# Performance work log

Measured on AMD Instinct MI355X. Metric: run time of the kernel, lower is better.

## Reference

```python
import jax, jax.numpy as jnp
import numpy as np

# Baked genome DAG structure (static per-instance in the original module)
N_IN = 256
LAYER_SIZES = [256, 256, 256, 256, 64]  # 4 hidden layers + output layer
N_OUT = LAYER_SIZES[-1]
N_EVAL = sum(LAYER_SIZES)  # 1088 eval nodes (node_evals)
DEG = 32                   # incoming links per eval node
BATCH = 8192


def setup_inputs() -> dict:
    key = jax.random.key(0)
    kx, kw, kb, kr = jax.random.split(key, 4)
    x = jax.random.normal(kx, (BATCH, N_IN), dtype=jnp.float32)
    # connection weights, node bias, node response (learned genome params)
    w = jax.random.normal(kw, (N_EVAL, DEG), dtype=jnp.float32) * 0.5
    bias = jax.random.normal(kb, (N_EVAL,), dtype=jnp.float32) * 0.1
    response = 1.0 + jax.random.normal(kr, (N_EVAL,), dtype=jnp.float32) * 0.1
    # per-layer source indices: each eval node connects to DEG earlier nodes
    src_rows = []
    offset = N_IN  # number of nodes topologically before current layer
    for li, sz in enumerate(LAYER_SIZES):
        ks = jax.random.fold_in(key, 100 + li)
        src_rows.append(jax.random.randint(ks, (sz, DEG), 0, offset, dtype=jnp.int32))
        offset += sz
    src_idx = jnp.concatenate(src_rows, axis=0)  # [N_EVAL, DEG]
    return {"x": x, "w": w, "bias": bias, "response": response, "src_idx": src_idx}


def reference(x, w, bias, response, src_idx):
    # values: [B, n_nodes_so_far]; starts as the input node values
    values = x
    row = 0
    for sz in LAYER_SIZES:  # small fixed structural loop (topological layers)
        s = src_idx[row:row + sz]                       # [sz, DEG]
        gathered = values[:, s]                         # [B, sz, DEG]
        agg = jnp.einsum('bsd,sd->bs', gathered, w[row:row + sz])  # sum aggregation
        out = jax.nn.relu(bias[row:row + sz] + response[row:row + sz] * agg)
        values = jnp.concatenate([values, out], axis=1)
        row += sz
    return values[:, -N_OUT:]  # [B, N_OUT]
```

## Files before the change

kernel.cpp:

```cpp
#include <hip/hip_runtime.h>

#define N_IN   256
#define N_EVAL 1088
#define TOTALW 1344
#define DEG    32

typedef __attribute__((ext_vector_type(8))) short short8;
typedef __attribute__((ext_vector_type(4))) float f32x4;
typedef unsigned short u16;
typedef unsigned int   u32;

__device__ __forceinline__ u32 pk2(float lo, float hi) {
    u32 ul = __float_as_uint(lo);
    u32 uh = __float_as_uint(hi);
    ul = (ul + 0x7fffu + ((ul >> 16) & 1u)) >> 16;
    uh = (uh + 0x7fffu + ((uh >> 16) & 1u)) & 0xffff0000u;
    return ul | uh;
}
__device__ __forceinline__ u16 bf1(float v) {
    u32 u = __float_as_uint(v);
    return (u16)((u + 0x7fffu + ((u >> 16) & 1u)) >> 16);
}

__global__ __launch_bounds__(256) void build_dense32(
    const int* __restrict__ src, const float* __restrict__ w,
    u32* __restrict__ B32)
{
    const int t = blockIdx.x * 256 + threadIdx.x;
    const int tile = t >> 8;
    const int q    = t & 255;
    const int lane = q >> 2;
    const int e2   = q & 3;
    int li, ts;
    if      (tile < 128)  { li = 0; ts = 0;    }
    else if (tile < 384)  { li = 1; ts = 128;  }
    else if (tile < 768)  { li = 2; ts = 384;  }
    else if (tile < 1280) { li = 3; ts = 768;  }
    else                  { li = 4; ts = 1280; }
    const int tloc = tile - ts;
    int kt, nt;
    if (li < 4) { kt = tloc >> 4; nt = tloc & 15; }
    else        { kt = tloc >> 2; nt = tloc & 3;  }
    const int ln = lane & 15, g = lane >> 4;
    const int gn = li * 256 + nt * 16 + ln;
    const int k0 = kt * 32 + g * 8 + e2 * 2;

    int c[DEG]; float ow[DEG];
    const int4*   s4 = (const int4*)(src + (size_t)gn * DEG);
    const float4* w4 = (const float4*)(w   + (size_t)gn * DEG);
    #pragma unroll
    for (int k = 0; k < 8; ++k) {
        int4 ci = s4[k]; float4 wf = w4[k];
        c[4*k+0]=ci.x; c[4*k+1]=ci.y; c[4*k+2]=ci.z; c[4*k+3]=ci.w;
        ow[4*k+0]=wf.x; ow[4*k+1]=wf.y; ow[4*k+2]=wf.z; ow[4*k+3]=wf.w;
    }
    float s0 = 0.f, s1 = 0.f;
    #pragma unroll
    for (int d = 0; d < DEG; ++d) {
        s0 += (c[d] == k0    ) ? ow[d] : 0.f;
        s1 += (c[d] == k0 + 1) ? ow[d] : 0.f;
    }
    B32[t] = pk2(s0, s1);
}

#define TILE_B 32
#define LDSCOLS 1280
#define RSTRIDE (LDSCOLS * 2)

#define MFMA(a, b, c) __builtin_amdgcn_mfma_f32_16x16x32_bf16(a, b, c, 0, 0, 0)

__global__ __launch_bounds__(512) void neat_mfma(
    const float* __restrict__ x, const u16* __restrict__ Bbuf,
    const float* __restrict__ bias, const float* __restrict__ resp,
    float* __restrict__ out)
{
    __shared__ uint4 ldsq[(TILE_B * RSTRIDE) / 16];
    __shared__ f32x4 pbuf[4 * 64 * 2];
    char* lds = (char*)ldsq;
    const int tid  = threadIdx.x;
    const int b0   = blockIdx.x * TILE_B;
    const int lane = tid & 63;
    const int wvid = tid >> 6;

    const short8* Bf = (const short8*)Bbuf;
    short8 rp0[8], rp1[8];
    {
        const short8* bp0 = Bf + wvid * 64 + lane;
        const short8* bp1 = Bf + (wvid + 8) * 64 + lane;
        #pragma unroll
        for (int j = 0; j < 8; ++j) {
            rp0[j] = bp0[j * 1024];
            rp1[j] = bp1[j * 1024];
        }
    }

    #pragma unroll
    for (int i = 0; i < 4; ++i) {
        int f4 = tid + i * 512;
        int row = f4 >> 6;
        int c4  = f4 & 63;
        float4 xv = ((const float4*)(x + (size_t)(b0 + row) * N_IN))[c4];
        u32 p0 = pk2(xv.x, xv.y), p1 = pk2(xv.z, xv.w);
        int byte = row * RSTRIDE + ((c4 * 8) ^ ((row & 7) << 4));
        *(u32*)(lds + byte)     = p0;
        *(u32*)(lds + byte + 4) = p1;
    }
    __syncthreads();

    const int r0  = lane & 15;
    const int g16 = (lane >> 4) << 4;
    const int sw  = (r0 & 7) << 4;
    const int ab0 = r0 * RSTRIDE;
    const int ab1 = (r0 + 16) * RSTRIDE;

    int cbase = N_IN;
    #pragma unroll
    for (int li = 0; li < 5; ++li) {
        const int ktn = (N_IN + li * 256) >> 5;
        const int loff8[5] = {0, 8192, 24576, 49152, 81920};
        const int lo8 = loff8[li];
        const int nbase = cbase - N_IN;

        if (li < 4) {
            const int STEP = 16 * 64;
            const int nt0 = wvid, nt1 = wvid + 8;
            const short8* bp0 = Bf + lo8 + nt0 * 64 + lane;
            const short8* bp1 = Bf + lo8 + nt1 * 64 + lane;
            if (li != 0) {
                #pragma unroll
                for (int j = 0; j < 8; ++j) {
                    rp0[j] = bp0[j * STEP];
                    rp1[j] = bp1[j * STEP];
                }
            }
            const int gr0 = nbase + nt0 * 16 + r0;
            const int gr1 = nbase + nt1 * 16 + r0;
            const float bb0 = bias[gr0], rr0 = resp[gr0];
            const float bb1 = bias[gr1], rr1 = resp[gr1];

            f32x4 acc00 = {0,0,0,0}, acc01 = {0,0,0,0};
            f32x4 acc10 = {0,0,0,0}, acc11 = {0,0,0,0};
            for (int kt8 = 0; kt8 < ktn; kt8 += 8) {
                #pragma unroll
                for (int j = 0; j < 8; ++j) {
                    int kt  = kt8 + j;
                    int ktp = kt + 8; if (ktp >= ktn) ktp = ktn - 1;
                    short8 f0 = bp0[ktp * STEP];
                    short8 f1 = bp1[ktp * STEP];
                    int inrow = (kt * 64 + g16) ^ sw;
                    short8 a0 = *(const short8*)(lds + ab0 + inrow);
                    short8 a1 = *(const short8*)(lds + ab1 + inrow);
                    acc00 = MFMA(a0, rp0[j], acc00);
                    acc01 = MFMA(a1, rp0[j], acc01);
                    acc10 = MFMA(a0, rp1[j], acc10);
                    acc11 = MFMA(a1, rp1[j], acc11);
                    rp0[j] = f0; rp1[j] = f1;
                }
            }
            #pragma unroll
            for (int t = 0; t < 2; ++t) {
                int nt = t ? nt1 : nt0;
                f32x4 aA = t ? acc10 : acc00;
                f32x4 aB = t ? acc11 : acc01;
                float bb = t ? bb1 : bb0;
                float rr = t ? rr1 : rr0;
                int colbyte = (cbase + nt * 16 + r0) * 2;
                #pragma unroll
                for (int r = 0; r < 4; ++r) {
                    int i0 = ((lane >> 4) << 2) + r;
                    float v0 = fmaxf(fmaf(rr, aA[r], bb), 0.f);
                    *(u16*)(lds + i0 * RSTRIDE + (colbyte ^ ((i0 & 7) << 4))) = bf1(v0);
                    int i1 = i0 + 16;
                    float v1 = fmaxf(fmaf(rr, aB[r], bb), 0.f);
                    *(u16*)(lds + i1 * RSTRIDE + (colbyte ^ ((i1 & 7) << 4))) = bf1(v1);
                }
            }
            __syncthreads();
        } else {
            const int STEP = 4 * 64;
            const int nt0   = wvid & 3;
            const int ktbeg = (wvid >> 2) * 20;
            const int ktend = ktbeg + 20;
            const short8* bp0 = Bf + lo8 + nt0 * 64 + lane;
            #pragma unroll
            for (int j = 0; j < 4; ++j) rp0[j] = bp0[(ktbeg + j) * STEP];
            const int gr0 = nbase + nt0 * 16 + r0;
            const float bb0 = bias[gr0], rr0 = resp[gr0];

            f32x4 acc0 = {0,0,0,0}, acc1 = {0,0,0,0};
            for (int kt4 = ktbeg; kt4 < ktend; kt4 += 4) {
                #pragma unroll
                for (int j = 0; j < 4; ++j) {
                    int kt  = kt4 + j;
                    int ktp = kt + 4; if (ktp >= ktend) ktp = ktend - 1;
                    short8 f0 = bp0[ktp * STEP];
                    int inrow = (kt * 64 + g16) ^ sw;
                    short8 a0 = *(const short8*)(lds + ab0 + inrow);
                    short8 a1 = *(const short8*)(lds + ab1 + inrow);
                    acc0 = MFMA(a0, rp0[j], acc0);
                    acc1 = MFMA(a1, rp0[j], acc1);
                    rp0[j] = f0;
                }
            }
            if (wvid >= 4) {
                pbuf[((wvid - 4) * 64 + lane) * 2 + 0] = acc0;
                pbuf[((wvid - 4) * 64 + lane) * 2 + 1] = acc1;
            }
            __syncthreads();
            if (wvid < 4) {
                f32x4 q0 = pbuf[(wvid * 64 + lane) * 2 + 0];
                f32x4 q1 = pbuf[(wvid * 64 + lane) * 2 + 1];
                acc0 += q0; acc1 += q1;
                int col = nt0 * 16 + r0;
                #pragma unroll
                for (int r = 0; r < 4; ++r) {
                    int i0 = ((lane >> 4) << 2) + r;
                    out[(size_t)(b0 + i0) * 64 + col] = fmaxf(fmaf(rr0, acc0[r], bb0), 0.f);
                    int i1 = i0 + 16;
                    out[(size_t)(b0 + i1) * 64 + col] = fmaxf(fmaf(rr0, acc1[r], bb0), 0.f);
                }
            }
        }
        cbase += 256;
    }
}

#define FTILE_B 16
__device__ __forceinline__ int gbyte(int c, int h) {
    return ((c << 5) + (h << 4)) ^ (int)((((unsigned)c >> 2) & 7u) << 5);
}
__device__ __forceinline__ void fmadw(u32 d, float wv, float* acc) {
    acc[0] = fmaf(__uint_as_float(d << 16), wv, acc[0]);
    acc[1] = fmaf(__uint_as_float(d & 0xffff0000u), wv, acc[1]);
}
__device__ __forceinline__ void colacc16(const u32* vals, int c, float wv, float* acc) {
    const uint4* p = (const uint4*)((const char*)vals + gbyte(c, 0));
    uint4 a = p[0]; uint4 b = p[1];
    fmadw(a.x, wv, acc + 0);  fmadw(a.y, wv, acc + 2);
    fmadw(a.z, wv, acc + 4);  fmadw(a.w, wv, acc + 6);
    fmadw(b.x, wv, acc + 8);  fmadw(b.y, wv, acc + 10);
    fmadw(b.z, wv, acc + 12); fmadw(b.w, wv, acc + 14);
}
__global__ __launch_bounds__(256) void neat_eval_r4(
    const float* __restrict__ x, const float* __restrict__ w,
    const float* __restrict__ bias, const float* __restrict__ resp,
    const int* __restrict__ src, float* __restrict__ out)
{
    __shared__ u32 vals[TOTALW * 8];
    const int tid = threadIdx.x;
    const int b0  = blockIdx.x * FTILE_B;
    #pragma unroll
    for (int i = 0; i < 2; ++i) {
        int g = tid + i * 256;
        int c = g & 255, h = g >> 8;
        u32 pk[4];
        #pragma unroll
        for (int j = 0; j < 4; ++j) {
            float lo = x[(size_t)(b0 + h * 8 + 2 * j    ) * N_IN + c];
            float hi = x[(size_t)(b0 + h * 8 + 2 * j + 1) * N_IN + c];
            pk[j] = pk2(lo, hi);
        }
        *(uint4*)((char*)vals + gbyte(c, h)) = make_uint4(pk[0], pk[1], pk[2], pk[3]);
    }
    __syncthreads();
    int row = 0, outoff = N_IN;
    #pragma unroll
    for (int li = 0; li < 5; ++li) {
        const int sz = (li < 4) ? 256 : 64;
        for (int n = tid; n < sz; n += 256) {
            const int gr = row + n;
            const int4*   s4 = (const int4*)(src + (size_t)gr * DEG);
            const float4* w4 = (const float4*)(w   + (size_t)gr * DEG);
            float acc[16];
            #pragma unroll
            for (int i = 0; i < 16; ++i) acc[i] = 0.f;
            #pragma unroll
            for (int k = 0; k < DEG / 4; ++k) {
                int4 i4 = s4[k]; float4 wv = w4[k];
                colacc16(vals, i4.x, wv.x, acc);
                colacc16(vals, i4.y, wv.y, acc);
                colacc16(vals, i4.z, wv.z, acc);
                colacc16(vals, i4.w, wv.w, acc);
            }
            const float bb = bias[gr], rr = resp[gr];
            u32 pk[8];
            #pragma unroll
            for (int j = 0; j < 8; ++j) {
                float lo = fmaxf(fmaf(rr, acc[2 * j    ], bb), 0.f);
                float hi = fmaxf(fmaf(rr, acc[2 * j + 1], bb), 0.f);
                pk[j] = pk2(lo, hi);
            }
            int ob = gbyte(outoff + n, 0);
            *(uint4*)((char*)vals + ob)      = make_uint4(pk[0], pk[1], pk[2], pk[3]);
            *(uint4*)((char*)vals + ob + 16) = make_uint4(pk[4], pk[5], pk[6], pk[7]);
        }
        __syncthreads();
        row += sz; outoff += sz;
    }
    #pragma unroll
    for (int i = 0; i < 4; ++i) {
        int idx = tid + i * 256;
        int c = idx & 63, b = idx >> 6;
        int col = TOTALW - 64 + c;
        const u32* g = (const u32*)((const char*)vals + gbyte(col, b >> 3));
        u32 d = g[(b & 7) >> 1];
        float v = (b & 1) ? __uint_as_float(d & 0xffff0000u)
                          : __uint_as_float(d << 16);
        out[(size_t)(b0 + b) * 64 + c] = v;
    }
}

extern "C" void kernel_launch(void* const* d_in, const int* in_sizes, int n_in,
                              void* d_out, int out_size, void* d_ws, size_t ws_size,
                              hipStream_t stream) {
    const float* x    = (const float*)d_in[0];
    const float* w    = (const float*)d_in[1];
    const float* bias = (const float*)d_in[2];
    const float* resp = (const float*)d_in[3];
    const int*   src  = (const int*)d_in[4];
    float* out = (float*)d_out;

    const int batch = in_sizes[0] / N_IN;
    const size_t need = 737280ull * 2;

    if (ws_size >= need && (batch % TILE_B) == 0) {
        u32* Bbuf = (u32*)d_ws;
        build_dense32<<<1440, 256, 0, stream>>>(src, w, Bbuf);
        neat_mfma<<<batch / TILE_B, 512, 0, stream>>>(x, (const u16*)Bbuf, bias, resp, out);
    } else {
        neat_eval_r4<<<batch / FTILE_B, 256, 0, stream>>>(x, w, bias, resp, src, out);
    }
}
```

Baseline: 29.56 us.

## Double batch tile to 64 rows with 1024-thread blocks and drop output split-K

Each block now handles 64 batch rows with 16 waves. Waves are split into two M-halves that share the same B-fragment column tiles, so each block loads the dense weight matrix once for twice as many rows. The output layer no longer splits K across waves and reduces through a shared buffer; each wave owns one 16x16 output tile over the full K range. The trade-off is LDS doubling to about 160KB per block, which allows only one block per CU, and half as many blocks (128) for 256 CUs, which risks leaving CUs idle.

```diff
diff --git a/kernel.cpp b/kernel.cpp
--- a/kernel.cpp
+++ b/kernel.cpp
@@ -63,30 +63,32 @@
     B32[t] = pk2(s0, s1);
 }
 
-#define TILE_B 32
+#define TILE_B 64
 #define LDSCOLS 1280
 #define RSTRIDE (LDSCOLS * 2)
 
 #define MFMA(a, b, c) __builtin_amdgcn_mfma_f32_16x16x32_bf16(a, b, c, 0, 0, 0)
 
-__global__ __launch_bounds__(512) void neat_mfma(
+__global__ __launch_bounds__(1024) void neat_mfma(
     const float* __restrict__ x, const u16* __restrict__ Bbuf,
     const float* __restrict__ bias, const float* __restrict__ resp,
     float* __restrict__ out)
 {
     __shared__ uint4 ldsq[(TILE_B * RSTRIDE) / 16];
-    __shared__ f32x4 pbuf[4 * 64 * 2];
     char* lds = (char*)ldsq;
     const int tid  = threadIdx.x;
     const int b0   = blockIdx.x * TILE_B;
     const int lane = tid & 63;
     const int wvid = tid >> 6;
 
+    const int np = wvid & 7;
+    const int mp = wvid >> 3;
+
     const short8* Bf = (const short8*)Bbuf;
     short8 rp0[8], rp1[8];
     {
-        const short8* bp0 = Bf + wvid * 64 + lane;
-        const short8* bp1 = Bf + (wvid + 8) * 64 + lane;
+        const short8* bp0 = Bf + np * 64 + lane;
+        const short8* bp1 = Bf + (np + 8) * 64 + lane;
         #pragma unroll
         for (int j = 0; j < 8; ++j) {
             rp0[j] = bp0[j * 1024];
@@ -96,7 +98,7 @@
 
     #pragma unroll
     for (int i = 0; i < 4; ++i) {
-        int f4 = tid + i * 512;
+        int f4 = tid + i * 1024;
         int row = f4 >> 6;
         int c4  = f4 & 63;
         float4 xv = ((const float4*)(x + (size_t)(b0 + row) * N_IN))[c4];
@@ -110,8 +112,8 @@
     const int r0  = lane & 15;
     const int g16 = (lane >> 4) << 4;
     const int sw  = (r0 & 7) << 4;
-    const int ab0 = r0 * RSTRIDE;
-    const int ab1 = (r0 + 16) * RSTRIDE;
+    const int ab0 = (r0 + mp * 32) * RSTRIDE;
+    const int ab1 = (r0 + 16 + mp * 32) * RSTRIDE;
 
     int cbase = N_IN;
     #pragma unroll
@@ -123,9 +125,8 @@
 
         if (li < 4) {
             const int STEP = 16 * 64;
-            const int nt0 = wvid, nt1 = wvid + 8;
-            const short8* bp0 = Bf + lo8 + nt0 * 64 + lane;
-            const short8* bp1 = Bf + lo8 + nt1 * 64 + lane;
+            const short8* bp0 = Bf + lo8 + np * 64 + lane;
+            const short8* bp1 = Bf + lo8 + (np + 8) * 64 + lane;
             if (li != 0) {
                 #pragma unroll
                 for (int j = 0; j < 8; ++j) {
@@ -133,8 +134,8 @@
                     rp1[j] = bp1[j * STEP];
                 }
             }
-            const int gr0 = nbase + nt0 * 16 + r0;
-            const int gr1 = nbase + nt1 * 16 + r0;
+            const int gr0 = nbase + np * 16 + r0;
+            const int gr1 = nbase + (np + 8) * 16 + r0;
             const float bb0 = bias[gr0], rr0 = resp[gr0];
             const float bb1 = bias[gr1], rr1 = resp[gr1];
 
@@ -159,7 +160,7 @@
             }
             #pragma unroll
             for (int t = 0; t < 2; ++t) {
-                int nt = t ? nt1 : nt0;
+                int nt = t ? (np + 8) : np;
                 f32x4 aA = t ? acc10 : acc00;
                 f32x4 aB = t ? acc11 : acc01;
                 float bb = t ? bb1 : bb0;
@@ -167,7 +168,7 @@
                 int colbyte = (cbase + nt * 16 + r0) * 2;
                 #pragma unroll
                 for (int r = 0; r < 4; ++r) {
-                    int i0 = ((lane >> 4) << 2) + r;
+                    int i0 = mp * 32 + ((lane >> 4) << 2) + r;
                     float v0 = fmaxf(fmaf(rr, aA[r], bb), 0.f);
                     *(u16*)(lds + i0 * RSTRIDE + (colbyte ^ ((i0 & 7) << 4))) = bf1(v0);
                     int i1 = i0 + 16;
@@ -178,47 +179,33 @@
             __syncthreads();
         } else {
             const int STEP = 4 * 64;
-            const int nt0   = wvid & 3;
-            const int ktbeg = (wvid >> 2) * 20;
-            const int ktend = ktbeg + 20;
-            const short8* bp0 = Bf + lo8 + nt0 * 64 + lane;
-            #pragma unroll
-            for (int j = 0; j < 4; ++j) rp0[j] = bp0[(ktbeg + j) * STEP];
-            const int gr0 = nbase + nt0 * 16 + r0;
+            const int mt = wvid >> 2;
+            const int nt = wvid & 3;
+            const int ab = (r0 + mt * 16) * RSTRIDE;
+            const short8* bp0 = Bf + lo8 + nt * 64 + lane;
+            #pragma unroll
+            for (int j = 0; j < 8; ++j) rp0[j] = bp0[j * STEP];
+            const int gr0 = nbase + nt * 16 + r0;
             const float bb0 = bias[gr0], rr0 = resp[gr0];
 
-            f32x4 acc0 = {0,0,0,0}, acc1 = {0,0,0,0};
-            for (int kt4 = ktbeg; kt4 < ktend; kt4 += 4) {
+            f32x4 acc0 = {0,0,0,0};
+            for (int kt8 = 0; kt8 < 40; kt8 += 8) {
                 #pragma unroll
-                for (int j = 0; j < 4; ++j) {
-                    int kt  = kt4 + j;
-                    int ktp = kt + 4; if (ktp >= ktend) ktp = ktend - 1;
+                for (int j = 0; j < 8; ++j) {
+                    int kt  = kt8 + j;
+                    int ktp = kt + 8; if (ktp >= 40) ktp = 39;
                     short8 f0 = bp0[ktp * STEP];
                     int inrow = (kt * 64 + g16) ^ sw;
-                    short8 a0 = *(const short8*)(lds + ab0 + inrow);
-                    short8 a1 = *(const short8*)(lds + ab1 + inrow);
+                    short8 a0 = *(const short8*)(lds + ab + inrow);
                     acc0 = MFMA(a0, rp0[j], acc0);
-                    acc1 = MFMA(a1, rp0[j], acc1);
                     rp0[j] = f0;
                 }
             }
-            if (wvid >= 4) {
-                pbuf[((wvid - 4) * 64 + lane) * 2 + 0] = acc0;
-                pbuf[((wvid - 4) * 64 + lane) * 2 + 1] = acc1;
-            }
-            __syncthreads();
-            if (wvid < 4) {
-                f32x4 q0 = pbuf[(wvid * 64 + lane) * 2 + 0];
-                f32x4 q1 = pbuf[(wvid * 64 + lane) * 2 + 1];
-                acc0 += q0; acc1 += q1;
-                int col = nt0 * 16 + r0;
-                #pragma unroll
-                for (int r = 0; r < 4; ++r) {
-                    int i0 = ((lane >> 4) << 2) + r;
-                    out[(size_t)(b0 + i0) * 64 + col] = fmaxf(fmaf(rr0, acc0[r], bb0), 0.f);
-                    int i1 = i0 + 16;
-                    out[(size_t)(b0 + i1) * 64 + col] = fmaxf(fmaf(rr0, acc1[r], bb0), 0.f);
-                }
+            int col = nt * 16 + r0;
+            #pragma unroll
+            for (int r = 0; r < 4; ++r) {
+                int i0 = mt * 16 + ((lane >> 4) << 2) + r;
+                out[(size_t)(b0 + i0) * 64 + col] = fmaxf(fmaf(rr0, acc0[r], bb0), 0.f);
             }
         }
         cbase += 256;
@@ -326,7 +313,7 @@
     if (ws_size >= need && (batch % TILE_B) == 0) {
         u32* Bbuf = (u32*)d_ws;
         build_dense32<<<1440, 256, 0, stream>>>(src, w, Bbuf);
-        neat_mfma<<<batch / TILE_B, 512, 0, stream>>>(x, (const u16*)Bbuf, bias, resp, out);
+        neat_mfma<<<batch / TILE_B, 1024, 0, stream>>>(x, (const u16*)Bbuf, bias, resp, out);
     } else {
         neat_eval_r4<<<batch / FTILE_B, 256, 0, stream>>>(x, w, bias, resp, src, out);
     }
```

New measurement: 42.00 us. 42.1% more time.

## Rotate per-block K start phase and prefetch next layer weights early

Applied to the files above, without the earlier changes.

Each block now starts its K-loop at an offset derived from the block id, so blocks fetch different weight slices at the same time instead of all hitting the same addresses. The first register fragments for the next layer are loaded before the epilogue and barrier of the current layer, hiding global load latency behind the epilogue. The cost is extra modulo and index arithmetic in the inner loop. A stray label was also added.

```diff
diff --git a/kernel.cpp b/kernel.cpp
--- a/kernel.cpp
+++ b/kernel.cpp
@@ -78,19 +78,22 @@
     __shared__ f32x4 pbuf[4 * 64 * 2];
     char* lds = (char*)ldsq;
     const int tid  = threadIdx.x;
-    const int b0   = blockIdx.x * TILE_B;
+    const int bid  = blockIdx.x;
+    const int b0   = bid * TILE_B;
     const int lane = tid & 63;
     const int wvid = tid >> 6;
 
     const short8* Bf = (const short8*)Bbuf;
     short8 rp0[8], rp1[8];
     {
+        const int rot0 = bid & 7;
         const short8* bp0 = Bf + wvid * 64 + lane;
         const short8* bp1 = Bf + (wvid + 8) * 64 + lane;
         #pragma unroll
         for (int j = 0; j < 8; ++j) {
-            rp0[j] = bp0[j * 1024];
-            rp1[j] = bp1[j * 1024];
+            int ph = j + rot0; if (ph >= 8) ph -= 8;
+            rp0[j] = bp0[ph * 1024];
+            rp1[j] = bp1[ph * 1024];
         }
     }
 
@@ -123,16 +126,10 @@
 
         if (li < 4) {
             const int STEP = 16 * 64;
+            const int rot  = bid % ktn;
             const int nt0 = wvid, nt1 = wvid + 8;
             const short8* bp0 = Bf + lo8 + nt0 * 64 + lane;
             const short8* bp1 = Bf + lo8 + nt1 * 64 + lane;
-            if (li != 0) {
-                #pragma unroll
-                for (int j = 0; j < 8; ++j) {
-                    rp0[j] = bp0[j * STEP];
-                    rp1[j] = bp1[j * STEP];
-                }
-            }
             const int gr0 = nbase + nt0 * 16 + r0;
             const int gr1 = nbase + nt1 * 16 + r0;
             const float bb0 = bias[gr0], rr0 = resp[gr0];
@@ -145,9 +142,11 @@
                 for (int j = 0; j < 8; ++j) {
                     int kt  = kt8 + j;
                     int ktp = kt + 8; if (ktp >= ktn) ktp = ktn - 1;
-                    short8 f0 = bp0[ktp * STEP];
-                    short8 f1 = bp1[ktp * STEP];
-                    int inrow = (kt * 64 + g16) ^ sw;
+                    int php = ktp + rot; if (php >= ktn) php -= ktn;
+                    short8 f0 = bp0[php * STEP];
+                    short8 f1 = bp1[php * STEP];
+                    int phk = kt + rot; if (phk >= ktn) phk -= ktn;
+                    int inrow = (phk * 64 + g16) ^ sw;
                     short8 a0 = *(const short8*)(lds + ab0 + inrow);
                     short8 a1 = *(const short8*)(lds + ab1 + inrow);
                     acc00 = MFMA(a0, rp0[j], acc00);
@@ -157,6 +156,30 @@
                     rp0[j] = f0; rp1[j] = f1;
                 }
             }
+
+            if (li < 3) {
+                const int ktnN = (N_IN + (li + 1) * 256) >> 5;
+                const int rotN = bid % ktnN;
+                const short8* bn0 = Bf + loff8[li + 1] + nt0 * 64 + lane;
+                const short8* bn1 = Bf + loff8[li + 1] + nt1 * 64 + lane;
+                #pragma unroll
+                for (int j = 0; j < 8; ++j) {
+                    int ph = j + rotN; if (ph >= ktnN) ph -= ktnN;
+                    rp0[j] = bn0[ph * STEP];
+                    rp1[j] = bn1[ph * STEP];
+                }
+            } else {
+                const int nt4   = wvid & 3;
+                const int ktbg4 = (wvid >> 2) * 20;
+                const int rot4  = bid % 20;
+                const short8* b4 = Bf + loff8[4] + nt4 * 64 + lane;
+                #pragma unroll
+                for (int j = 0; j < 4; ++j) {
+                    int ph = j + rot4; if (ph >= 20) ph -= 20;
+                    rp0[j] = b4[(ktbg4 + ph) * 256];
+                }
+            }
+
             #pragma unroll
             for (int t = 0; t < 2; ++t) {
                 int nt = t ? nt1 : nt0;
@@ -180,24 +203,25 @@
             const int STEP = 4 * 64;
             const int nt0   = wvid & 3;
             const int ktbeg = (wvid >> 2) * 20;
-            const int ktend = ktbeg + 20;
+            const int rot4  = bid % 20;
             const short8* bp0 = Bf + lo8 + nt0 * 64 + lane;
-            #pragma unroll
-            for (int j = 0; j < 4; ++j) rp0[j] = bp0[(ktbeg + j) * STEP];
             const int gr0 = nbase + nt0 * 16 + r0;
             const float bb0 = bias[gr0], rr0 = resp[gr0];
 
             f32x4 acc0 = {0,0,0,0}, acc1 = {0,0,0,0};
-            for (int kt4 = ktbeg; kt4 < ktend; kt4 += 4) {
+            for (int kt4 = 0; kt4 < 20; kt4 += 4) {
                 #pragma unroll
                 for (int j = 0; j < 4; ++j) {
-                    int kt  = kt4 + j;
-                    int ktp = kt + 4; if (ktp >= ktend) ktp = ktend - 1;
-                    short8 f0 = bp0[ktp * STEP];
-                    int inrow = (kt * 64 + g16) ^ sw;
+                    int lcl  = kt4 + j;
+                    int lclp = lcl + 4; if (lclp >= 20) lclp = 19;
+                    int php = lclp + rot4; if (php >= 20) php -= 20;
+                    short8 f0 = bp0[(ktbeg + php) * STEP];
+                    int phk = lcl + rot4; if (phk >= 20) phk -= 20;
+                    int inrow = ((ktbeg + phk) * 64 + g16) ^ sw;
                     short8 a0 = *(const short8*)(lds + ab0 + inrow);
                     short8 a1 = *(const short8*)(lds + ab1 + inrow);
                     acc0 = MFMA(a0, rp0[j], acc0);
+                    ac1:;
                     acc1 = MFMA(a1, rp0[j], acc1);
                     rp0[j] = f0;
                 }
```

Measured after the change: 27.40 us. 7.3% less time.
